# Kernel tuning notes

Measured on AMD Instinct MI355X. Metric: run time of the kernel, lower is better.

## Reference

```python
import jax, jax.numpy as jnp
import numpy as np

B, C, P, E, M, H, K = 1024, 8192, 3, 64, 128, 16, 8
SCALE = 0.05
EPS = 1e-12  # tf.math.l2_normalize epsilon


def setup_inputs() -> dict:
    key = jax.random.key(0)
    ks = jax.random.split(key, 16)
    return {
        'pools': jax.random.uniform(ks[0], (B, C), dtype=jnp.float32),            # dense stand-in for SparseTensor batch_pools
        'metapaths': jax.random.uniform(ks[1], (P, C, C), dtype=jnp.float32),     # card-card metapath matrices
        'card_embeddings': jax.random.normal(ks[2], (C, E), dtype=jnp.float32) * SCALE,
        'mp_kernels': jax.random.normal(ks[3], (P, E, M), dtype=jnp.float32) * SCALE,
        'mp_biases': jnp.zeros((P, M, 1), dtype=jnp.float32),
        'Wq': jax.random.normal(ks[4], (M, H, K), dtype=jnp.float32) * SCALE,
        'bq': jnp.zeros((H, K), dtype=jnp.float32),
        'Wk': jax.random.normal(ks[5], (M, H, K), dtype=jnp.float32) * SCALE,
        'bk': jnp.zeros((H, K), dtype=jnp.float32),
        'Wv': jax.random.normal(ks[6], (M, H, K), dtype=jnp.float32) * SCALE,
        'bv': jnp.zeros((H, K), dtype=jnp.float32),
        'Wo': jax.random.normal(ks[7], (H, K, M), dtype=jnp.float32) * SCALE,
        'bo': jnp.zeros((M,), dtype=jnp.float32),
        'pool_kernel': jax.random.normal(ks[8], (M, E), dtype=jnp.float32) * SCALE,
        'pool_bias': jnp.zeros((E,), dtype=jnp.float32),
    }


def _l2_normalize(x, axis):
    # matches tf.math.l2_normalize: x / sqrt(max(sum(x^2), eps))
    sq = jnp.sum(jnp.square(x), axis=axis, keepdims=True)
    return x * jax.lax.rsqrt(jnp.maximum(sq, EPS))


def reference(pools, metapaths, card_embeddings, mp_kernels, mp_biases,
              Wq, bq, Wk, bk, Wv, bv, Wo, bo, pool_kernel, pool_bias):
    # --- MetapathEmbed layers, vectorized over the P metapaths ---
    # path_card_embeddings: act(einsum('ce,em->mc') + bias) -> (P, M, C)
    path_card = jax.nn.silu(jnp.einsum('ce,pem->pmc', card_embeddings, mp_kernels) + mp_biases)
    # path_card_matrix: einsum('mc,cd->dm') -> (P, C, M)
    pcm = jnp.einsum('pmc,pcd->pdm', path_card, metapaths)
    # sparse_dense_matmul(batch_pools, path_card_matrix); stack over metapaths -> (B, P, M)
    x = jnp.einsum('bd,pdm->bpm', pools, pcm)

    # --- keras MultiHeadAttention(query=x, value=x) ---
    q = jnp.einsum('bpm,mhk->bphk', x, Wq) + bq
    k = jnp.einsum('bpm,mhk->bphk', x, Wk) + bk
    v = jnp.einsum('bpm,mhk->bphk', x, Wv) + bv
    scores = jnp.einsum('bphk,bqhk->bhpq', q, k) / np.float32(np.sqrt(K))
    attn = jax.nn.softmax(scores, axis=-1)
    o = jnp.einsum('bhpq,bqhk->bphk', attn, v)
    attended = jnp.einsum('bphk,hkm->bpm', o, Wo) + bo  # (B, P, M)

    # --- pooling head ---
    pre_pool = jnp.sum(attended, axis=1)                       # (B, M)
    pool_embeds = jnp.einsum('bm,me->be', pre_pool, pool_kernel) + pool_bias
    norm_pool = _l2_normalize(pool_embeds, axis=1)             # (B, E)
    norm_cards = _l2_normalize(card_embeddings, axis=1)        # (C, E)
    return (jnp.einsum('be,ce->bc', norm_pool, norm_cards) + 1.0) / 2.0
```

## Files before the change

### kernel.cpp

```cpp
#include <hip/hip_runtime.h>
#include <hip/hip_bf16.h>

typedef unsigned int uint;
typedef unsigned short ushort;
typedef float f32x4 __attribute__((ext_vector_type(4)));
typedef short s16x8 __attribute__((ext_vector_type(8)));
typedef int i32x4 __attribute__((ext_vector_type(4)));
typedef uint u32x2 __attribute__((ext_vector_type(2)));

#define C_DIM 8192
#define B_DIM 1024
#define P_DIM 3
#define E_DIM 64
#define M_DIM 128

#define PCA_OFF   0ull
#define PART_OFF  15728640ull
#define PCMH_OFF  66060288ull
#define PCML_OFF  72351744ull
#define XPART_OFF PART_OFF
#define NPOOL_OFF 78643200ull
#define NCARD_OFF 78774272ull

__device__ __forceinline__ uint bf16_rne(float f) {
  uint u = __builtin_bit_cast(uint, f);
  return (u + 0x7fffu + ((u >> 16) & 1u)) >> 16;
}
__device__ __forceinline__ float bf16_to_f32(uint b) {
  return __builtin_bit_cast(float, b << 16);
}
__device__ __forceinline__ uint pk2(float a, float b) {
  float2 t; t.x = a; t.y = b;
  __hip_bfloat162 h2 = __float22bfloat162_rn(t);
  uint r;
  __builtin_memcpy(&r, &h2, 4);
  return r;
}
__device__ __forceinline__ void glds16(const void* gsrc, void* ldst) {
  __builtin_amdgcn_global_load_lds(
      (const __attribute__((address_space(1))) uint*)gsrc,
      (__attribute__((address_space(3))) uint*)ldst, 16, 0, 0);
}

__global__ __launch_bounds__(256) void k1_pathcard(
    const float* __restrict__ cardemb, const float* __restrict__ mpk,
    const float* __restrict__ mpbias, ushort* __restrict__ pcA) {
  __shared__ float ce_l[64 * 68];
  const int tid = threadIdx.x;
  const int cb = blockIdx.x;
  const int p  = blockIdx.y;
  for (int r = 0; r < 16; ++r) {
    int i = r * 256 + tid;
    int row = i >> 6, col = i & 63;
    ce_l[row * 68 + col] = cardemb[(size_t)(cb * 64 + row) * 64 + col];
  }
  __syncthreads();
  const int m = tid & 127;
  const int chalf = tid >> 7;
  float kr[64];
#pragma unroll
  for (int e = 0; e < 64; ++e) kr[e] = mpk[(size_t)p * E_DIM * M_DIM + e * M_DIM + m];
  const float bias = mpbias[p * M_DIM + m];
  for (int cl0 = 0; cl0 < 32; ++cl0) {
    int cl = chalf * 32 + cl0;
    float acc = bias;
#pragma unroll
    for (int e = 0; e < 64; ++e) acc += ce_l[cl * 68 + e] * kr[e];
    float s = acc / (1.0f + expf(-acc));
    uint hb = bf16_rne(s);
    uint lb = bf16_rne(s - bf16_to_f32(hb));
    int c = cb * 64 + cl;
    int kt = c >> 5, kl = c & 31;
    size_t off = ((size_t)(p * 256 + kt) * 20480 + (size_t)m * 80 + (size_t)kl * 2) >> 1;
    pcA[off] = (ushort)hb;
    pcA[off + 5120] = (ushort)lb;
  }
}

__global__ __launch_bounds__(256, 2) void k2_big(
    const float* __restrict__ mp, const ushort* __restrict__ pcA,
    float* __restrict__ partial) {
  extern __shared__ char smem[];
  const int tid = threadIdx.x;
  int lin = blockIdx.x + 64 * (blockIdx.y + 4 * blockIdx.z);
  int swz = (lin & 7) * 96 + (lin >> 3);
  const int dt = swz & 63, q = (swz >> 6) & 3, p = swz >> 8;
  const int lane = tid & 63, wid = tid >> 6;
  const int wr = wid >> 1, wc = wid & 1;
  const int r16 = lane & 15, g4 = lane >> 4;
  const float* mpb = mp + (size_t)p * C_DIM * C_DIM + (size_t)dt * 128;
  const char* pcb = (const char*)pcA + (size_t)(p * 256 + q * 64) * 20480;
  const int sd = tid & 127, skh = tid >> 7;
  const int fc = ((sd ^ (sd >> 2)) & 3) << 4;
  const int fr = ((r16 ^ (r16 >> 2)) & 3) << 4;

  f32x4 acc[4][4];
#pragma unroll
  for (int i = 0; i < 4; ++i)
#pragma unroll
    for (int j = 0; j < 4; ++j) acc[i][j] = (f32x4){0.f, 0.f, 0.f, 0.f};

  auto stageA = [&](int t, int buf) {
    const char* src = pcb + (size_t)t * 20480;
    char* dst = smem + buf * 20480;
#pragma unroll
    for (int r = 0; r < 5; ++r)
      glds16(src + r * 4096 + wid * 1024 + lane * 16, dst + r * 4096 + wid * 1024);
  };
  auto loadB = [&](int t, float* br) {
    int c0 = q * 2048 + t * 32;
#pragma unroll
    for (int ii = 0; ii < 2; ++ii) {
      const float* rp = mpb + (size_t)(c0 + ii * 16 + skh * 8) * C_DIM + sd;
#pragma unroll
      for (int j = 0; j < 8; ++j) br[ii * 8 + j] = rp[(size_t)j * C_DIM];
    }
  };
  auto writeB = [&](const float* br, int buf) {
    char* bb = smem + 40960 + buf * 16384;
#pragma unroll
    for (int ii = 0; ii < 2; ++ii) {
      uint hw[4], lw[4];
#pragma unroll
      for (int k2 = 0; k2 < 4; ++k2) {
        float v0 = br[ii * 8 + k2 * 2], v1 = br[ii * 8 + k2 * 2 + 1];
        uint h = pk2(v0, v1);
        float h0 = __builtin_bit_cast(float, h << 16);
        float h1 = __builtin_bit_cast(float, h & 0xffff0000u);
        hw[k2] = h;
        lw[k2] = pk2(v0 - h0, v1 - h1);
      }
      int off = sd * 64 + ((((ii * 2 + skh) << 4)) ^ fc);
      *(i32x4*)(bb + off) = (i32x4){(int)hw[0], (int)hw[1], (int)hw[2], (int)hw[3]};
      *(i32x4*)(bb + 8192 + off) = (i32x4){(int)lw[0], (int)lw[1], (int)lw[2], (int)lw[3]};
    }
  };
  auto compute = [&](int buf) {
    const char* Ab = smem + buf * 20480;
    const char* Bb = smem + 40960 + buf * 16384;
    s16x8 ah[4], al[4], bh[4], bl[4];
#pragma unroll
    for (int i = 0; i < 4; ++i) {
      int off = (wr * 64 + i * 16 + r16) * 80 + g4 * 16;
      ah[i] = *(const s16x8*)(Ab + off);
      al[i] = *(const s16x8*)(Ab + 10240 + off);
    }
#pragma unroll
    for (int j = 0; j < 4; ++j) {
      int off = (wc * 64 + j * 16 + r16) * 64 + ((g4 << 4) ^ fr);
      bh[j] = *(const s16x8*)(Bb + off);
      bl[j] = *(const s16x8*)(Bb + 8192 + off);
    }
#pragma unroll
    for (int i = 0; i < 4; ++i)
#pragma unroll
      for (int j = 0; j < 4; ++j) {
        acc[i][j] = __builtin_amdgcn_mfma_f32_16x16x32_bf16(ah[i], bh[j], acc[i][j], 0, 0, 0);
        acc[i][j] = __builtin_amdgcn_mfma_f32_16x16x32_bf16(ah[i], bl[j], acc[i][j], 0, 0, 0);
        acc[i][j] = __builtin_amdgcn_mfma_f32_16x16x32_bf16(al[i], bh[j], acc[i][j], 0, 0, 0);
      }
  };

  float brA[16], brB[16];
  stageA(0, 0);
  asm volatile("" ::: "memory");
  loadB(0, brA);
  loadB(1, brB);
  writeB(brA, 0);
  asm volatile("s_waitcnt vmcnt(16)" ::: "memory");
  asm volatile("s_waitcnt lgkmcnt(0)" ::: "memory");
  __builtin_amdgcn_s_barrier();

#define K2_STEP(T, BUFC, BRW, BRL, TAIL)                                      \
  {                                                                           \
    if (!(TAIL)) {                                                            \
      stageA((T) + 1, 1 - (BUFC));                                            \
      asm volatile("" ::: "memory");                                          \
      int tnn = (T) + 2 < 64 ? (T) + 2 : 63;                                  \
      loadB(tnn, BRL);                                                        \
    }                                                                         \
    compute(BUFC);                                                            \
    if (!(TAIL)) {                                                            \
      writeB(BRW, 1 - (BUFC));                                                \
      asm volatile("s_waitcnt vmcnt(16)" ::: "memory");                       \
      asm volatile("s_waitcnt lgkmcnt(0)" ::: "memory");                      \
      __builtin_amdgcn_s_barrier();                                           \
    }                                                                         \
  }

  for (int t2 = 0; t2 < 32; ++t2) {
    int t = 2 * t2;
    K2_STEP(t, 0, brB, brA, false);
    K2_STEP(t + 1, 1, brA, brB, (t2 == 31));
  }
#undef K2_STEP

  float* part = partial + (size_t)(q * 3 + p) * M_DIM * C_DIM + (size_t)dt * 128;
#pragma unroll
  for (int i = 0; i < 4; ++i)
#pragma unroll
    for (int j = 0; j < 4; ++j)
#pragma unroll
      for (int r = 0; r < 4; ++r)
        part[(size_t)(wr * 64 + i * 16 + g4 * 4 + r) * C_DIM + (wc * 64 + j * 16 + r16)] =
            acc[i][j][r];
}

__global__ __launch_bounds__(256) void k2b_reduce(const float* __restrict__ p0,
                                                  ushort* __restrict__ oh,
                                                  ushort* __restrict__ ol) {
  size_t i = (size_t)blockIdx.x * 256 + threadIdx.x;
  f32x4 a = *(const f32x4*)(p0 + i * 4);
  f32x4 b = *(const f32x4*)(p0 + 3145728ull + i * 4);
  f32x4 c = *(const f32x4*)(p0 + 6291456ull + i * 4);
  f32x4 d = *(const f32x4*)(p0 + 9437184ull + i * 4);
  f32x4 s = (a + b) + (c + d);
  uint h[2], l[2];
#pragma unroll
  for (int k = 0; k < 2; ++k) {
    float v0 = s[k * 2], v1 = s[k * 2 + 1];
    uint hh = pk2(v0, v1);
    float h0 = __builtin_bit_cast(float, hh << 16);
    float h1 = __builtin_bit_cast(float, hh & 0xffff0000u);
    h[k] = hh;
    l[k] = pk2(v0 - h0, v1 - h1);
  }
  *(u32x2*)(oh + i * 4) = (u32x2){h[0], h[1]};
  *(u32x2*)(ol + i * 4) = (u32x2){l[0], l[1]};
}

__global__ __launch_bounds__(256, 2) void k3_x(const float* __restrict__ pools,
                                               const ushort* __restrict__ pcmh,
                                               const ushort* __restrict__ pcml,
                                               float* __restrict__ xpart) {
  const int tid = threadIdx.x;
  const int bt = blockIdx.x, ks = blockIdx.y;
  const int lane = tid & 63, wid = tid >> 6;
  const int wr = wid >> 1, wc = wid & 1;
  const int r16 = lane & 15, g4 = lane >> 4;
  const int rowbase = bt * 64 + wr * 32;
  f32x4 a0[2][4], a1[2][4], a2[2][4];
#pragma unroll
  for (int i = 0; i < 2; ++i)
#pragma unroll
    for (int j = 0; j < 4; ++j) {
      a0[i][j] = (f32x4){0.f, 0.f, 0.f, 0.f};
      a1[i][j] = (f32x4){0.f, 0.f, 0.f, 0.f};
      a2[i][j] = (f32x4){0.f, 0.f, 0.f, 0.f};
    }

  for (int t = 0; t < 16; ++t) {
    int d0 = ks * 512 + t * 32 + g4 * 8;
    s16x8 ah[2], al[2];
#pragma unroll
    for (int i = 0; i < 2; ++i) {
      const float* ap = pools + (size_t)(rowbase + i * 16 + r16) * C_DIM + d0;
      f32x4 v0 = *(const f32x4*)ap;
      f32x4 v1 = *(const f32x4*)(ap + 4);
      i32x4 hw, lw;
#pragma unroll
      for (int k2 = 0; k2 < 4; ++k2) {
        float x0 = (k2 < 2) ? v0[k2 * 2] : v1[(k2 - 2) * 2];
        float x1 = (k2 < 2) ? v0[k2 * 2 + 1] : v1[(k2 - 2) * 2 + 1];
        uint h = pk2(x0, x1);
        float h0 = __builtin_bit_cast(float, h << 16);
        float h1 = __builtin_bit_cast(float, h & 0xffff0000u);
        hw[k2] = (int)h;
        lw[k2] = (int)pk2(x0 - h0, x1 - h1);
      }
      ah[i] = __builtin_bit_cast(s16x8, hw);
      al[i] = __builtin_bit_cast(s16x8, lw);
    }
    auto do_p = [&](f32x4(*acc)[4], int p) {
#pragma unroll
      for (int j = 0; j < 4; ++j) {
        size_t boff = (size_t)(p * M_DIM + wc * 64 + j * 16 + r16) * C_DIM + d0;
        s16x8 bh = *(const s16x8*)(pcmh + boff);
        s16x8 bl = *(const s16x8*)(pcml + boff);
#pragma unroll
        for (int i = 0; i < 2; ++i) {
          acc[i][j] = __builtin_amdgcn_mfma_f32_16x16x32_bf16(ah[i], bh, acc[i][j], 0, 0, 0);
          acc[i][j] = __builtin_amdgcn_mfma_f32_16x16x32_bf16(ah[i], bl, acc[i][j], 0, 0, 0);
          acc[i][j] = __builtin_amdgcn_mfma_f32_16x16x32_bf16(al[i], bh, acc[i][j], 0, 0, 0);
        }
      }
    };
    do_p(a0, 0);
    do_p(a1, 1);
    do_p(a2, 2);
  }
  auto store_p = [&](f32x4(*acc)[4], int p) {
#pragma unroll
    for (int i = 0; i < 2; ++i)
#pragma unroll
      for (int j = 0; j < 4; ++j)
#pragma unroll
        for (int r = 0; r < 4; ++r) {
          int row = rowbase + i * 16 + g4 * 4 + r;
          xpart[((size_t)(ks * B_DIM + row) * 3 + p) * M_DIM + wc * 64 + j * 16 + r16] =
              acc[i][j][r];
        }
  };
  store_p(a0, 0);
  store_p(a1, 1);
  store_p(a2, 2);
}

__global__ __launch_bounds__(128) void k4_attn(
    const float* __restrict__ xpart, const float* __restrict__ Wq,
    const float* __restrict__ bq, const float* __restrict__ Wk,
    const float* __restrict__ bk, const float* __restrict__ Wv,
    const float* __restrict__ bv, const float* __restrict__ Wo,
    const float* __restrict__ bo, const float* __restrict__ pk,
    const float* __restrict__ pb, ushort* __restrict__ npool) {
  __shared__ float xs[3 * 128], qa[3 * 128], ka[3 * 128], va[3 * 128], oa[3 * 128], pp[128];
  const int t = threadIdx.x;
  const int b = blockIdx.x;
#pragma unroll
  for (int p = 0; p < 3; ++p) {
    float v = 0.f;
    for (int ks = 0; ks < 16; ++ks)
      v += xpart[((size_t)(ks * B_DIM + b) * 3 + p) * M_DIM + t];
    xs[p * 128 + t] = v;
  }
  __syncthreads();
  float qv[3], kv[3], vv[3];
#pragma unroll
  for (int p = 0; p < 3; ++p) { qv[p] = bq[t]; kv[p] = bk[t]; vv[p] = bv[t]; }
  for (int m = 0; m < 128; ++m) {
    float wq = Wq[m * 128 + t], wk = Wk[m * 128 + t], wv = Wv[m * 128 + t];
#pragma unroll
    for (int p = 0; p < 3; ++p) {
      float xv = xs[p * 128 + m];
      qv[p] += xv * wq;
      kv[p] += xv * wk;
      vv[p] += xv * wv;
    }
  }
#pragma unroll
  for (int p = 0; p < 3; ++p) {
    qa[p * 128 + t] = qv[p];
    ka[p * 128 + t] = kv[p];
    va[p * 128 + t] = vv[p];
  }
  __syncthreads();
  const int h = t >> 3;
  float w[3][3];
#pragma unroll
  for (int p = 0; p < 3; ++p) {
    float s[3];
#pragma unroll
    for (int qq = 0; qq < 3; ++qq) {
      float d = 0.f;
#pragma unroll
      for (int kk = 0; kk < 8; ++kk)
        d += qa[p * 128 + h * 8 + kk] * ka[qq * 128 + h * 8 + kk];
      s[qq] = d / 2.8284271247461903f;
    }
    float mx = fmaxf(s[0], fmaxf(s[1], s[2]));
    float e0 = expf(s[0] - mx), e1 = expf(s[1] - mx), e2 = expf(s[2] - mx);
    float inv = 1.0f / (e0 + e1 + e2);
    w[p][0] = e0 * inv; w[p][1] = e1 * inv; w[p][2] = e2 * inv;
  }
#pragma unroll
  for (int p = 0; p < 3; ++p) {
    float o = w[p][0] * va[0 * 128 + t] + w[p][1] * va[1 * 128 + t] + w[p][2] * va[2 * 128 + t];
    oa[p * 128 + t] = o;
  }
  __syncthreads();
  float pre = 3.0f * bo[t];
#pragma unroll
  for (int p = 0; p < 3; ++p)
    for (int hk = 0; hk < 128; ++hk) pre += oa[p * 128 + hk] * Wo[hk * 128 + t];
  pp[t] = pre;
  __syncthreads();
  if (t < 64) {
    float pe = pb[t];
    for (int m = 0; m < 128; ++m) pe += pp[m] * pk[m * 64 + t];
    float ss = pe * pe;
#pragma unroll
    for (int off = 32; off; off >>= 1) ss += __shfl_xor(ss, off, 64);
    float rs = 1.0f / sqrtf(fmaxf(ss, 1e-12f));
    npool[b * 64 + t] = (ushort)bf16_rne(pe * rs);
  }
}

__global__ __launch_bounds__(256) void k4b_ncard(const float* __restrict__ ce,
                                                 ushort* __restrict__ ncard) {
  const int t = threadIdx.x;
  const int r = blockIdx.x * 4 + (t >> 6);
  const int lane = t & 63;
  float v = ce[(size_t)r * 64 + lane];
  float ss = v * v;
#pragma unroll
  for (int off = 32; off; off >>= 1) ss += __shfl_xor(ss, off, 64);
  float rs = 1.0f / sqrtf(fmaxf(ss, 1e-12f));
  ncard[(size_t)r * 64 + lane] = (ushort)bf16_rne(v * rs);
}

__global__ __launch_bounds__(256, 2) void k5_out(const ushort* __restrict__ np_,
                                                 const ushort* __restrict__ nc,
                                                 float* __restrict__ out) {
  const int tid = threadIdx.x;
  const int bt = blockIdx.x, ct = blockIdx.y;
  const int lane = tid & 63, wid = tid >> 6;
  const int wr = wid >> 1, wc = wid & 1;
  const int r16 = lane & 15, g4 = lane >> 4;
  f32x4 acc[4][4];
#pragma unroll
  for (int i = 0; i < 4; ++i)
#pragma unroll
    for (int j = 0; j < 4; ++j) acc[i][j] = (f32x4){0.f, 0.f, 0.f, 0.f};
#pragma unroll
  for (int ks = 0; ks < 2; ++ks) {
    int e0 = ks * 32 + g4 * 8;
    s16x8 af[4], bf_[4];
#pragma unroll
    for (int i = 0; i < 4; ++i)
      af[i] = *(const s16x8*)(np_ + (size_t)(bt * 128 + wr * 64 + i * 16 + r16) * 64 + e0);
#pragma unroll
    for (int j = 0; j < 4; ++j)
      bf_[j] = *(const s16x8*)(nc + (size_t)(ct * 128 + wc * 64 + j * 16 + r16) * 64 + e0);
#pragma unroll
    for (int i = 0; i < 4; ++i)
#pragma unroll
      for (int j = 0; j < 4; ++j)
        acc[i][j] = __builtin_amdgcn_mfma_f32_16x16x32_bf16(af[i], bf_[j], acc[i][j], 0, 0, 0);
  }
#pragma unroll
  for (int i = 0; i < 4; ++i)
#pragma unroll
    for (int j = 0; j < 4; ++j)
#pragma unroll
      for (int r = 0; r < 4; ++r) {
        int row = bt * 128 + wr * 64 + i * 16 + g4 * 4 + r;
        int col = ct * 128 + wc * 64 + j * 16 + r16;
        out[(size_t)row * C_DIM + col] = (acc[i][j][r] + 1.0f) * 0.5f;
      }
}

extern "C" void kernel_launch(void* const* d_in, const int* in_sizes, int n_in,
                              void* d_out, int out_size, void* d_ws, size_t ws_size,
                              hipStream_t stream) {
  const float* pools = (const float*)d_in[0];
  const float* metapaths = (const float*)d_in[1];
  const float* cardemb = (const float*)d_in[2];
  const float* mpk = (const float*)d_in[3];
  const float* mpbias = (const float*)d_in[4];
  const float* Wq = (const float*)d_in[5];
  const float* bq = (const float*)d_in[6];
  const float* Wk = (const float*)d_in[7];
  const float* bk = (const float*)d_in[8];
  const float* Wv = (const float*)d_in[9];
  const float* bv = (const float*)d_in[10];
  const float* Wo = (const float*)d_in[11];
  const float* bo = (const float*)d_in[12];
  const float* pk = (const float*)d_in[13];
  const float* pb = (const float*)d_in[14];
  float* out = (float*)d_out;
  char* ws = (char*)d_ws;

  ushort* pcA = (ushort*)(ws + PCA_OFF);
  float* part = (float*)(ws + PART_OFF);
  ushort* pcmh = (ushort*)(ws + PCMH_OFF);
  ushort* pcml = (ushort*)(ws + PCML_OFF);
  float* xpart = (float*)(ws + XPART_OFF);
  ushort* npool = (ushort*)(ws + NPOOL_OFF);
  ushort* ncard = (ushort*)(ws + NCARD_OFF);

  k1_pathcard<<<dim3(128, 3), dim3(256), 0, stream>>>(cardemb, mpk, mpbias, pcA);
  k2_big<<<dim3(64, 4, 3), dim3(256), 73728, stream>>>(metapaths, pcA, part);
  k2b_reduce<<<dim3(3072), dim3(256), 0, stream>>>(part, pcmh, pcml);
  k3_x<<<dim3(16, 16), dim3(256), 0, stream>>>(pools, pcmh, pcml, xpart);
  k4b_ncard<<<dim3(2048), dim3(256), 0, stream>>>(cardemb, ncard);
  k4_attn<<<dim3(1024), dim3(128), 0, stream>>>(xpart, Wq, bq, Wk, bk, Wv, bv, Wo, bo, pk, pb,
                                                npool);
  k5_out<<<dim3(8, 64), dim3(256), 0, stream>>>(npool, ncard, out);
}
```

Before: 402.7 us.

## Read k2 A-operand directly from global, shrink LDS, retile k3 over merged P columns

k2_big stops staging the pre-split bf16 path-card A tiles into LDS and loads its MFMA fragments straight from global memory. That frees LDS (static 32 KB instead of 72 KB dynamic) so occupancy can rise to 3 blocks per CU, and sched barriers are added around the B-tile sync. k3_x is retiled to 32-row blocks with each wave covering 96 of the 384 concatenated P×M columns, doubling the grid, and the next pools tile is prefetched into registers. The risk is that uncached global loads of A in k2's inner loop add latency that LDS staging used to hide.

```diff
diff --git a/kernel.cpp b/kernel.cpp
--- a/kernel.cpp
+++ b/kernel.cpp
@@ -35,11 +35,6 @@
   uint r;
   __builtin_memcpy(&r, &h2, 4);
   return r;
-}
-__device__ __forceinline__ void glds16(const void* gsrc, void* ldst) {
-  __builtin_amdgcn_global_load_lds(
-      (const __attribute__((address_space(1))) uint*)gsrc,
-      (__attribute__((address_space(3))) uint*)ldst, 16, 0, 0);
 }
 
 __global__ __launch_bounds__(256) void k1_pathcard(
@@ -77,10 +72,10 @@
   }
 }
 
-__global__ __launch_bounds__(256, 2) void k2_big(
+__global__ __launch_bounds__(256, 3) void k2_big(
     const float* __restrict__ mp, const ushort* __restrict__ pcA,
     float* __restrict__ partial) {
-  extern __shared__ char smem[];
+  __shared__ char smem[32768];
   const int tid = threadIdx.x;
   int lin = blockIdx.x + 64 * (blockIdx.y + 4 * blockIdx.z);
   int swz = (lin & 7) * 96 + (lin >> 3);
@@ -100,13 +95,6 @@
 #pragma unroll
     for (int j = 0; j < 4; ++j) acc[i][j] = (f32x4){0.f, 0.f, 0.f, 0.f};
 
-  auto stageA = [&](int t, int buf) {
-    const char* src = pcb + (size_t)t * 20480;
-    char* dst = smem + buf * 20480;
-#pragma unroll
-    for (int r = 0; r < 5; ++r)
-      glds16(src + r * 4096 + wid * 1024 + lane * 16, dst + r * 4096 + wid * 1024);
-  };
   auto loadB = [&](int t, float* br) {
     int c0 = q * 2048 + t * 32;
 #pragma unroll
@@ -117,7 +105,7 @@
     }
   };
   auto writeB = [&](const float* br, int buf) {
-    char* bb = smem + 40960 + buf * 16384;
+    char* bb = smem + buf * 16384;
 #pragma unroll
     for (int ii = 0; ii < 2; ++ii) {
       uint hw[4], lw[4];
@@ -135,15 +123,15 @@
       *(i32x4*)(bb + 8192 + off) = (i32x4){(int)lw[0], (int)lw[1], (int)lw[2], (int)lw[3]};
     }
   };
-  auto compute = [&](int buf) {
-    const char* Ab = smem + buf * 20480;
-    const char* Bb = smem + 40960 + buf * 16384;
+  auto compute = [&](int t, int buf) {
+    const char* At = pcb + (size_t)t * 20480;
+    const char* Bb = smem + buf * 16384;
     s16x8 ah[4], al[4], bh[4], bl[4];
 #pragma unroll
     for (int i = 0; i < 4; ++i) {
       int off = (wr * 64 + i * 16 + r16) * 80 + g4 * 16;
-      ah[i] = *(const s16x8*)(Ab + off);
-      al[i] = *(const s16x8*)(Ab + 10240 + off);
+      ah[i] = *(const s16x8*)(At + off);
+      al[i] = *(const s16x8*)(At + 10240 + off);
     }
 #pragma unroll
     for (int j = 0; j < 4; ++j) {
@@ -162,38 +150,31 @@
   };
 
   float brA[16], brB[16];
-  stageA(0, 0);
-  asm volatile("" ::: "memory");
   loadB(0, brA);
   loadB(1, brB);
   writeB(brA, 0);
-  asm volatile("s_waitcnt vmcnt(16)" ::: "memory");
   asm volatile("s_waitcnt lgkmcnt(0)" ::: "memory");
   __builtin_amdgcn_s_barrier();
-
-#define K2_STEP(T, BUFC, BRW, BRL, TAIL)                                      \
+  __builtin_amdgcn_sched_barrier(0);
+
+#define K2S(T, BRL, BRW, TAIL)                                                \
   {                                                                           \
+    if ((T) < 62) loadB((T) + 2, BRL);                                        \
+    compute((T), (T) & 1);                                                    \
     if (!(TAIL)) {                                                            \
-      stageA((T) + 1, 1 - (BUFC));                                            \
-      asm volatile("" ::: "memory");                                          \
-      int tnn = (T) + 2 < 64 ? (T) + 2 : 63;                                  \
-      loadB(tnn, BRL);                                                        \
-    }                                                                         \
-    compute(BUFC);                                                            \
-    if (!(TAIL)) {                                                            \
-      writeB(BRW, 1 - (BUFC));                                                \
-      asm volatile("s_waitcnt vmcnt(16)" ::: "memory");                       \
+      writeB(BRW, ((T) + 1) & 1);                                             \
       asm volatile("s_waitcnt lgkmcnt(0)" ::: "memory");                      \
       __builtin_amdgcn_s_barrier();                                           \
+      __builtin_amdgcn_sched_barrier(0);                                      \
     }                                                                         \
   }
 
   for (int t2 = 0; t2 < 32; ++t2) {
     int t = 2 * t2;
-    K2_STEP(t, 0, brB, brA, false);
-    K2_STEP(t + 1, 1, brA, brB, (t2 == 31));
-  }
-#undef K2_STEP
+    K2S(t, brA, brB, false);
+    K2S(t + 1, brB, brA, (t2 == 31));
+  }
+#undef K2S
 
   float* part = partial + (size_t)(q * 3 + p) * M_DIM * C_DIM + (size_t)dt * 128;
 #pragma unroll
@@ -235,33 +216,33 @@
                                                float* __restrict__ xpart) {
   const int tid = threadIdx.x;
   const int bt = blockIdx.x, ks = blockIdx.y;
-  const int lane = tid & 63, wid = tid >> 6;
-  const int wr = wid >> 1, wc = wid & 1;
+  const int lane = tid & 63, w = tid >> 6;
   const int r16 = lane & 15, g4 = lane >> 4;
-  const int rowbase = bt * 64 + wr * 32;
-  f32x4 a0[2][4], a1[2][4], a2[2][4];
+  const int rowbase = bt * 32;
+  f32x4 acc[2][6];
 #pragma unroll
   for (int i = 0; i < 2; ++i)
 #pragma unroll
-    for (int j = 0; j < 4; ++j) {
-      a0[i][j] = (f32x4){0.f, 0.f, 0.f, 0.f};
-      a1[i][j] = (f32x4){0.f, 0.f, 0.f, 0.f};
-      a2[i][j] = (f32x4){0.f, 0.f, 0.f, 0.f};
-    }
+    for (int j = 0; j < 6; ++j) acc[i][j] = (f32x4){0.f, 0.f, 0.f, 0.f};
+
+  f32x4 pv0[2], pv1[2];
+#pragma unroll
+  for (int i = 0; i < 2; ++i) {
+    const float* ap = pools + (size_t)(rowbase + i * 16 + r16) * C_DIM + ks * 512 + g4 * 8;
+    pv0[i] = *(const f32x4*)ap;
+    pv1[i] = *(const f32x4*)(ap + 4);
+  }
 
   for (int t = 0; t < 16; ++t) {
     int d0 = ks * 512 + t * 32 + g4 * 8;
     s16x8 ah[2], al[2];
 #pragma unroll
     for (int i = 0; i < 2; ++i) {
-      const float* ap = pools + (size_t)(rowbase + i * 16 + r16) * C_DIM + d0;
-      f32x4 v0 = *(const f32x4*)ap;
-      f32x4 v1 = *(const f32x4*)(ap + 4);
       i32x4 hw, lw;
 #pragma unroll
       for (int k2 = 0; k2 < 4; ++k2) {
-        float x0 = (k2 < 2) ? v0[k2 * 2] : v1[(k2 - 2) * 2];
-        float x1 = (k2 < 2) ? v0[k2 * 2 + 1] : v1[(k2 - 2) * 2 + 1];
+        float x0 = (k2 < 2) ? pv0[i][k2 * 2] : pv1[i][(k2 - 2) * 2];
+        float x1 = (k2 < 2) ? pv0[i][k2 * 2 + 1] : pv1[i][(k2 - 2) * 2 + 1];
         uint h = pk2(x0, x1);
         float h0 = __builtin_bit_cast(float, h << 16);
         float h1 = __builtin_bit_cast(float, h & 0xffff0000u);
@@ -271,39 +252,40 @@
       ah[i] = __builtin_bit_cast(s16x8, hw);
       al[i] = __builtin_bit_cast(s16x8, lw);
     }
-    auto do_p = [&](f32x4(*acc)[4], int p) {
-#pragma unroll
-      for (int j = 0; j < 4; ++j) {
-        size_t boff = (size_t)(p * M_DIM + wc * 64 + j * 16 + r16) * C_DIM + d0;
-        s16x8 bh = *(const s16x8*)(pcmh + boff);
-        s16x8 bl = *(const s16x8*)(pcml + boff);
-#pragma unroll
-        for (int i = 0; i < 2; ++i) {
-          acc[i][j] = __builtin_amdgcn_mfma_f32_16x16x32_bf16(ah[i], bh, acc[i][j], 0, 0, 0);
-          acc[i][j] = __builtin_amdgcn_mfma_f32_16x16x32_bf16(ah[i], bl, acc[i][j], 0, 0, 0);
-          acc[i][j] = __builtin_amdgcn_mfma_f32_16x16x32_bf16(al[i], bh, acc[i][j], 0, 0, 0);
-        }
-      }
-    };
-    do_p(a0, 0);
-    do_p(a1, 1);
-    do_p(a2, 2);
-  }
-  auto store_p = [&](f32x4(*acc)[4], int p) {
-#pragma unroll
-    for (int i = 0; i < 2; ++i)
-#pragma unroll
-      for (int j = 0; j < 4; ++j)
-#pragma unroll
-        for (int r = 0; r < 4; ++r) {
-          int row = rowbase + i * 16 + g4 * 4 + r;
-          xpart[((size_t)(ks * B_DIM + row) * 3 + p) * M_DIM + wc * 64 + j * 16 + r16] =
-              acc[i][j][r];
-        }
-  };
-  store_p(a0, 0);
-  store_p(a1, 1);
-  store_p(a2, 2);
+    if (t < 15) {
+#pragma unroll
+      for (int i = 0; i < 2; ++i) {
+        const float* ap =
+            pools + (size_t)(rowbase + i * 16 + r16) * C_DIM + d0 + 32;
+        pv0[i] = *(const f32x4*)ap;
+        pv1[i] = *(const f32x4*)(ap + 4);
+      }
+    }
+#pragma unroll
+    for (int j = 0; j < 6; ++j) {
+      int col = w * 96 + j * 16 + r16;
+      size_t boff = (size_t)col * C_DIM + d0;
+      s16x8 bh = *(const s16x8*)(pcmh + boff);
+      s16x8 bl = *(const s16x8*)(pcml + boff);
+#pragma unroll
+      for (int i = 0; i < 2; ++i) {
+        acc[i][j] = __builtin_amdgcn_mfma_f32_16x16x32_bf16(ah[i], bh, acc[i][j], 0, 0, 0);
+        acc[i][j] = __builtin_amdgcn_mfma_f32_16x16x32_bf16(ah[i], bl, acc[i][j], 0, 0, 0);
+        acc[i][j] = __builtin_amdgcn_mfma_f32_16x16x32_bf16(al[i], bh, acc[i][j], 0, 0, 0);
+      }
+    }
+  }
+#pragma unroll
+  for (int i = 0; i < 2; ++i)
+#pragma unroll
+    for (int j = 0; j < 6; ++j)
+#pragma unroll
+      for (int r = 0; r < 4; ++r) {
+        int row = rowbase + i * 16 + g4 * 4 + r;
+        int col = w * 96 + j * 16 + r16;
+        int p = col >> 7, m = col & 127;
+        xpart[((size_t)(ks * B_DIM + row) * 3 + p) * M_DIM + m] = acc[i][j][r];
+      }
 }
 
 __global__ __launch_bounds__(128) void k4_attn(
@@ -469,9 +451,9 @@
   ushort* ncard = (ushort*)(ws + NCARD_OFF);
 
   k1_pathcard<<<dim3(128, 3), dim3(256), 0, stream>>>(cardemb, mpk, mpbias, pcA);
-  k2_big<<<dim3(64, 4, 3), dim3(256), 73728, stream>>>(metapaths, pcA, part);
+  k2_big<<<dim3(64, 4, 3), dim3(256), 0, stream>>>(metapaths, pcA, part);
   k2b_reduce<<<dim3(3072), dim3(256), 0, stream>>>(part, pcmh, pcml);
-  k3_x<<<dim3(16, 16), dim3(256), 0, stream>>>(pools, pcmh, pcml, xpart);
+  k3_x<<<dim3(32, 16), dim3(256), 0, stream>>>(pools, pcmh, pcml, xpart);
   k4b_ncard<<<dim3(2048), dim3(256), 0, stream>>>(cardemb, ncard);
   k4_attn<<<dim3(1024), dim3(128), 0, stream>>>(xpart, Wq, bq, Wk, bk, Wv, bv, Wo, bo, pk, pb,
                                                 npool);
```

After: 384.8 us. 1.05x faster.
